# Kernel optimization log

Measured on AMD Instinct MI355X. Metric: run time of the kernel, lower is better.

## Reference

```python
import jax, jax.numpy as jnp
import numpy as np

INPUT_SIZE = 512
LABEL_NUM = 8
OUTPUT_SIZE = 64
H1 = 1024  # shared bottom width
H2 = 512   # expert hidden width
B = 8192


def setup_inputs() -> dict:
    key = jax.random.key(0)
    ks = jax.random.split(key, 8)
    s_in = 1.0 / np.sqrt(INPUT_SIZE)
    s_h1 = 1.0 / np.sqrt(H1)
    s_h2 = 1.0 / np.sqrt(H2)
    return {
        "input": jax.random.normal(ks[0], (B, INPUT_SIZE), dtype=jnp.float32),
        "category": jax.random.randint(ks[1], (B,), 0, LABEL_NUM, dtype=jnp.int32),
        # shared bottom Linear(input_size, 1024): stored as [in, out]
        "W_in": jax.random.uniform(ks[2], (INPUT_SIZE, H1), jnp.float32, -s_in, s_in),
        "b_in": jax.random.uniform(ks[3], (H1,), jnp.float32, -s_in, s_in),
        # per-expert Linear(1024, 512) stacked over experts
        "W1": jax.random.uniform(ks[4], (LABEL_NUM, H1, H2), jnp.float32, -s_h1, s_h1),
        "b1": jax.random.uniform(ks[5], (LABEL_NUM, H2), jnp.float32, -s_h1, s_h1),
        # per-expert Linear(512, output_size) stacked over experts
        "W2": jax.random.uniform(ks[6], (LABEL_NUM, H2, OUTPUT_SIZE), jnp.float32, -s_h2, s_h2),
        "b2": jax.random.uniform(ks[7], (LABEL_NUM, OUTPUT_SIZE), jnp.float32, -s_h2, s_h2),
    }


def reference(input, category, W_in, b_in, W1, b1, W2, b2):
    # Shared bottom: Linear + ELU -> [B, H1]
    mid = jax.nn.elu(input @ W_in + b_in)
    # Run all experts densely, then hard-select per-sample expert output.
    # (Faithful to per-sample hard routing; small expert count makes this clean.)
    h = jax.nn.elu(jnp.einsum("bd,edh->beh", mid, W1) + b1[None, :, :])  # [B,E,H2]
    out_all = jnp.einsum("beh,eho->beo", h, W2) + b2[None, :, :]          # [B,E,O]
    # gather the chosen expert's output for each sample
    out = jnp.take_along_axis(out_all, category[:, None, None].astype(jnp.int32).repeat(1, axis=1), axis=1)
    return out[:, 0, :]  # [B, O]
```

## Files before the change

### kernel.cpp

```cpp
#include <hip/hip_runtime.h>

typedef unsigned short u16;
typedef unsigned int u32;
typedef __bf16 bf16x8 __attribute__((ext_vector_type(8)));
typedef float f32x4 __attribute__((ext_vector_type(4)));

#define GLD_LDS(gptr, lptr) \
  __builtin_amdgcn_global_load_lds((const __attribute__((address_space(1))) void*)(gptr), \
                                   (__attribute__((address_space(3))) void*)(lptr), 16, 0, 0)

__device__ __forceinline__ u16 f2b(float f) {
  union { __bf16 h; u16 u; } v; v.h = (__bf16)f; return v.u;
}
__device__ __forceinline__ float elu1(float v) {
  return v > 0.f ? v : (__expf(v) - 1.f);
}

__device__ void transpose_tile(float (*tbuf)[65], const float* __restrict__ src,
                               u16* __restrict__ dst, int R, int C, int tr, int tc,
                               size_t zoff) {
  const int tid = threadIdx.x;
  const float* sp = src + zoff + (size_t)(tr * 64) * C + tc * 64;
#pragma unroll
  for (int i = 0; i < 4; i++) {
    const int rr = (tid >> 4) + i * 16, f = tid & 15;
    float4 v = *reinterpret_cast<const float4*>(sp + (size_t)rr * C + f * 4);
    tbuf[rr][f * 4 + 0] = v.x; tbuf[rr][f * 4 + 1] = v.y;
    tbuf[rr][f * 4 + 2] = v.z; tbuf[rr][f * 4 + 3] = v.w;
  }
  __syncthreads();
  u16* dp = dst + zoff + (size_t)(tc * 64) * R + tr * 64;
#pragma unroll
  for (int i = 0; i < 4; i++) {
    const int u = tid + i * 256;
    const int c = u >> 4, rq = u & 15;
    ushort4 w;
    w.x = f2b(tbuf[rq * 4 + 0][c]); w.y = f2b(tbuf[rq * 4 + 1][c]);
    w.z = f2b(tbuf[rq * 4 + 2][c]); w.w = f2b(tbuf[rq * 4 + 3][c]);
    *reinterpret_cast<ushort4*>(dp + (size_t)c * R + rq * 4) = w;
  }
}

__device__ void hist_body(int rb, const int* __restrict__ cat, int* __restrict__ cnts) {
  __shared__ int c8[8];
  const int tid = threadIdx.x;
  if (tid < 8) c8[tid] = 0;
  __syncthreads();
  if (tid < 128) atomicAdd(&c8[cat[rb * 128 + tid]], 1);
  __syncthreads();
  if (tid < 8) cnts[rb * 8 + tid] = c8[tid];
}

__device__ void scatter_body(int rb, const int* __restrict__ cat,
                             const int* __restrict__ cnts,
                             int* __restrict__ list, int* __restrict__ off) {
  __shared__ int lc[512];
  __shared__ int lcur[8];
  __shared__ int starts[8];
  const int tid = threadIdx.x;
  lc[tid] = cnts[tid];
  lc[tid + 256] = cnts[tid + 256];
  if (tid < 8) lcur[tid] = 0;
  __syncthreads();
  if (tid < 8) {
    const int c = tid;
    int base = 0;
    for (int cc = 0; cc < c; cc++) {
      int s = 0;
      for (int b = 0; b < 64; b++) s += lc[b * 8 + cc];
      base += s;
    }
    int pre = 0;
    for (int b = 0; b < rb; b++) pre += lc[b * 8 + c];
    starts[c] = base + pre;
    if (rb == 0) {
      off[c] = base;
      if (c == 7) {
        int s = 0;
        for (int b = 0; b < 64; b++) s += lc[b * 8 + 7];
        off[8] = base + s;
      }
    }
  }
  __syncthreads();
  if (tid < 128) {
    const int idx = rb * 128 + tid;
    const int c = cat[idx];
    const int r = atomicAdd(&lcur[c], 1);
    list[starts[c] + r] = idx;
  }
}

__global__ __launch_bounds__(256) void wsmall(const float* __restrict__ W_in,
                                              const int* __restrict__ cat,
                                              const float* __restrict__ b2,
                                              u16* __restrict__ o0, int* __restrict__ cnts,
                                              float* __restrict__ out) {
  __shared__ float tbuf[64][65];
  const int bid = blockIdx.x, tid = threadIdx.x;
  if (bid >= 192) {
    const int r = (bid - 192) * 32 + (tid >> 3);
    const int co = (tid & 7) * 8;
    const int c = cat[r];
    float4 v0 = *reinterpret_cast<const float4*>(b2 + c * 64 + co);
    float4 v1 = *reinterpret_cast<const float4*>(b2 + c * 64 + co + 4);
    *reinterpret_cast<float4*>(out + (size_t)r * 64 + co) = v0;
    *reinterpret_cast<float4*>(out + (size_t)r * 64 + co + 4) = v1;
    return;
  }
  if (bid >= 128) { hist_body(bid - 128, cat, cnts); return; }
  transpose_tile(tbuf, W_in, o0, 512, 1024, bid >> 4, bid & 15, 0);
}


template<int LAYER, int BN, int K, int N>
__global__ __launch_bounds__(256, 4) void gemm_t(
    const float* __restrict__ Xf, const u16* __restrict__ A,
    const u16* __restrict__ Bw, const float* __restrict__ bias,
    const int* __restrict__ list, const int* __restrict__ off,
    u16* __restrict__ outb, float* __restrict__ outf,
    const int* __restrict__ cat, const int* __restrict__ cnts,
    int* __restrict__ wlist, int* __restrict__ woff,
    const float* __restrict__ Wc1, const float* __restrict__ Wc2,
    u16* __restrict__ o1, u16* __restrict__ o2) {
  struct GBuf { alignas(16) u16 As[2][2048]; alignas(16) u16 Bs[2][BN * 32]; };
  __shared__ union SM {
    GBuf g;
    float tbuf[64][65];
    u16 ht[64 * 136];
  } sm;

  const int tid = threadIdx.x;

  if constexpr (LAYER == 1) {
    if (blockIdx.y == 8) {
      if (blockIdx.x < 64) scatter_body(blockIdx.x, cat, cnts, wlist, woff);
      return;
    }
    if (blockIdx.y >= 9) {
      if (blockIdx.y <= 16) {
        const int t = (blockIdx.y - 9) * 128 + blockIdx.x;
        const int z = t >> 7, rem = t & 127;
        transpose_tile(sm.tbuf, Wc1, o1, 1024, 512, rem >> 3, rem & 7,
                       (size_t)z * 1024 * 512);
      } else if (blockIdx.x < 64) {
        const int t = blockIdx.x, z = t >> 3;
        transpose_tile(sm.tbuf, Wc2, o2, 512, 64, t & 7, 0, (size_t)z * 512 * 64);
      }
      return;
    }
  }

  int tidx, col0;
  if constexpr (LAYER == 1) {
    const int orig = blockIdx.y * 128 + blockIdx.x;
    const int work = (orig & 7) * 128 + (orig >> 3);
    tidx = work >> 3;
    col0 = (work & 7) * BN;
  } else {
    const int orig = blockIdx.y * 136 + blockIdx.x;
    const int work = (orig & 7) * 68 + (orig >> 3);
    tidx = work >> 2;
    col0 = (work & 3) * BN;
  }

  const int wave = tid >> 6, lane = tid & 63;

  int e = 0, start = 0, cnt = 0, rowbase;
  if constexpr (LAYER == 1) {
    rowbase = tidx * 64;
  } else {
    int t = tidx;
    int found = -1;
    for (e = 0; e < 8; e++) {
      int tiles = (off[e + 1] - off[e] + 63) >> 6;
      if (t < tiles) { found = e; break; }
      t -= tiles;
    }
    if (found < 0) return;
    start = off[e];
    cnt = off[e + 1] - start;
    rowbase = t * 64;
  }

  const int srow = tid >> 2, skc = tid & 3;
  const int kxs = (skc ^ (srow & 3)) * 8;

  const float* ax = nullptr;
  const u16* a_src = nullptr;
  if constexpr (LAYER == 1) {
    ax = Xf + (size_t)(rowbase + srow) * K + kxs;
  } else {
    int gr = list[start + min(rowbase + srow, cnt - 1)];
    a_src = A + (size_t)gr * K + kxs;
  }
  const u16* Bbase = Bw + (LAYER == 1 ? (size_t)0 : (size_t)e * N * K);
  const u16* b_src0 = Bbase + (size_t)(col0 + srow) * K + kxs;
  const u16* b_src1 = Bbase + (size_t)(col0 + 64 + srow) * K + kxs;

  const int wbase = wave * 512;

  constexpr int NR = BN / 32;
  const int wy = wave & 1, wx = wave >> 1;
  const int fr = lane & 15, kg = lane >> 4;
  const int kx = (kg ^ (fr & 3)) * 8;
  const int ar0 = (wy * 32 + fr) * 32 + kx;
  const int br0 = (wx * (BN / 2) + fr) * 32 + kx;

  f32x4 acc[2][NR] = {};

  float4 va0, va1;
  auto LOAD_A1 = [&](int t) {
    va0 = *reinterpret_cast<const float4*>(ax + t * 32);
    va1 = *reinterpret_cast<const float4*>(ax + t * 32 + 4);
  };
  auto WRITE_A1 = [&](int buf) {
    uint4 w;
    w.x = (u32)f2b(va0.x) | ((u32)f2b(va0.y) << 16);
    w.y = (u32)f2b(va0.z) | ((u32)f2b(va0.w) << 16);
    w.z = (u32)f2b(va1.x) | ((u32)f2b(va1.y) << 16);
    w.w = (u32)f2b(va1.z) | ((u32)f2b(va1.w) << 16);
    *reinterpret_cast<uint4*>(&sm.g.As[buf][srow * 32 + skc * 8]) = w;
  };
  auto COMPUTE = [&](int buf) {
    bf16x8 af[2], bfv[NR];
#pragma unroll
    for (int m = 0; m < 2; m++) af[m] = *(const bf16x8*)&sm.g.As[buf][ar0 + m * 16 * 32];
#pragma unroll
    for (int n = 0; n < NR; n++) bfv[n] = *(const bf16x8*)&sm.g.Bs[buf][br0 + n * 16 * 32];
#pragma unroll
    for (int m = 0; m < 2; m++)
#pragma unroll
      for (int n = 0; n < NR; n++)
        acc[m][n] = __builtin_amdgcn_mfma_f32_16x16x32_bf16(af[m], bfv[n], acc[m][n], 0, 0, 0);
  };

  constexpr int NK = K / 32;
  if constexpr (LAYER == 1) LOAD_A1(0);
  else GLD_LDS(a_src, &sm.g.As[0][wbase]);
  GLD_LDS(b_src0, &sm.g.Bs[0][wbase]);
  if constexpr (BN == 128) GLD_LDS(b_src1, &sm.g.Bs[0][2048 + wbase]);
  if constexpr (LAYER == 1) WRITE_A1(0);
  __syncthreads();

  for (int it = 0; it < NK; ++it) {
    const int cur = it & 1;
    const int nxt = cur ^ 1;
    if (it + 1 < NK) {
      const int kt = (it + 1) * 32;
      if constexpr (LAYER == 1) LOAD_A1(it + 1);
      else GLD_LDS(a_src + kt, &sm.g.As[nxt][wbase]);
      GLD_LDS(b_src0 + kt, &sm.g.Bs[nxt][wbase]);
      if constexpr (BN == 128) GLD_LDS(b_src1 + kt, &sm.g.Bs[nxt][2048 + wbase]);
    }
    COMPUTE(cur);
    if constexpr (LAYER == 1) { if (it + 1 < NK) WRITE_A1(nxt); }
    __syncthreads();
  }

  if constexpr (LAYER == 1) {
#pragma unroll
    for (int n = 0; n < NR; n++) {
      const int col = col0 + wx * (BN / 2) + n * 16 + fr;
      const float bc = bias[col];
#pragma unroll
      for (int m = 0; m < 2; m++) {
        const int rloc = wy * 32 + m * 16 + kg * 4;
#pragma unroll
        for (int j = 0; j < 4; j++)
          outb[(size_t)(rowbase + rloc + j) * N + col] = f2b(elu1(acc[m][n][j] + bc));
      }
    }
  } else {
#pragma unroll
    for (int n = 0; n < NR; n++) {
      const int lcol = wx * 64 + n * 16 + fr;
      const float bc = bias[e * N + col0 + lcol];
#pragma unroll
      for (int m = 0; m < 2; m++) {
        const int rl = wy * 32 + m * 16 + kg * 4;
#pragma unroll
        for (int j = 0; j < 4; j++)
          sm.ht[(rl + j) * 136 + lcol] = f2b(elu1(acc[m][n][j] + bc));
      }
    }
    __syncthreads();

    const u16* w2p = o2 + (size_t)e * 64 * 512 + col0;
    f32x4 po[2][2] = {};
#pragma unroll
    for (int ks = 0; ks < 4; ks++) {
      bf16x8 pa[2], pb[2];
#pragma unroll
      for (int m = 0; m < 2; m++)
        pa[m] = *(const bf16x8*)&sm.ht[(wy * 32 + m * 16 + fr) * 136 + ks * 32 + kg * 8];
#pragma unroll
      for (int n = 0; n < 2; n++)
        pb[n] = *(const bf16x8*)&w2p[(size_t)(wx * 32 + n * 16 + fr) * 512 + ks * 32 + kg * 8];
#pragma unroll
      for (int m = 0; m < 2; m++)
#pragma unroll
        for (int n = 0; n < 2; n++)
          po[m][n] = __builtin_amdgcn_mfma_f32_16x16x32_bf16(pa[m], pb[n], po[m][n], 0, 0, 0);
    }
#pragma unroll
    for (int n = 0; n < 2; n++) {
      const int oc = wx * 32 + n * 16 + fr;
#pragma unroll
      for (int m = 0; m < 2; m++) {
        const int sl0 = rowbase + wy * 32 + m * 16 + kg * 4;
#pragma unroll
        for (int j = 0; j < 4; j++) {
          const int slot = sl0 + j;
          if (slot < cnt)
            atomicAdd(&outf[(size_t)list[start + slot] * 64 + oc], po[m][n][j]);
        }
      }
    }
  }
}


extern "C" void kernel_launch(void* const* d_in, const int* in_sizes, int n_in,
                              void* d_out, int out_size, void* d_ws, size_t ws_size,
                              hipStream_t stream) {
  const float* x    = (const float*)d_in[0];
  const int*   cat  = (const int*)d_in[1];
  const float* W_in = (const float*)d_in[2];
  const float* b_in = (const float*)d_in[3];
  const float* W1   = (const float*)d_in[4];
  const float* b1   = (const float*)d_in[5];
  const float* W2   = (const float*)d_in[6];
  const float* b2   = (const float*)d_in[7];
  float* out = (float*)d_out;

  char* p = (char*)d_ws;
  u16* midb = (u16*)p; p += (size_t)8192 * 1024 * 2;
  u16* wtin = (u16*)p; p += (size_t)1024 * 512 * 2;
  u16* w1t  = (u16*)p; p += (size_t)8 * 512 * 1024 * 2;
  u16* w2t  = (u16*)p; p += (size_t)8 * 64 * 512 * 2;
  int* list = (int*)p; p += (size_t)8192 * 4;
  int* off  = (int*)p; p += 64;
  int* cnts = (int*)p; p += 64 * 8 * 4;

  wsmall<<<448, 256, 0, stream>>>(W_in, cat, b2, wtin, cnts, out);

  gemm_t<1, 128, 512, 1024><<<dim3(128, 18), 256, 0, stream>>>(
      x, nullptr, wtin, b_in, nullptr, nullptr, midb, nullptr,
      cat, cnts, list, off, W1, W2, w1t, w2t);

  gemm_t<2, 128, 1024, 512><<<dim3(136, 4), 256, 0, stream>>>(
      nullptr, midb, w1t, b1, list, off, nullptr, out,
      nullptr, nullptr, nullptr, nullptr, nullptr, nullptr, nullptr, w2t);
}
```

Baseline: 59.73 us.

## Shrink layer-2 tile to 64 columns and move bias init into layer-1 kernel

The layer-2 expert GEMM now uses 64-column tiles instead of 128, splitting each expert row tile into 8 column blocks over a 1D grid of 1088 blocks, with the fused second projection reducing over 64 hidden columns per block. The output bias-initialization work moves from the small prep kernel into extra blocks of the layer-1 kernel. Smaller tiles mean more blocks for better load balance and occupancy, at the cost of more partial-output accumulation into the output, less B reuse, and extra atomics.

```diff
diff --git a/kernel.cpp b/kernel.cpp
--- a/kernel.cpp
+++ b/kernel.cpp
@@ -93,21 +93,9 @@
 
 __global__ __launch_bounds__(256) void wsmall(const float* __restrict__ W_in,
                                               const int* __restrict__ cat,
-                                              const float* __restrict__ b2,
-                                              u16* __restrict__ o0, int* __restrict__ cnts,
-                                              float* __restrict__ out) {
+                                              u16* __restrict__ o0, int* __restrict__ cnts) {
   __shared__ float tbuf[64][65];
-  const int bid = blockIdx.x, tid = threadIdx.x;
-  if (bid >= 192) {
-    const int r = (bid - 192) * 32 + (tid >> 3);
-    const int co = (tid & 7) * 8;
-    const int c = cat[r];
-    float4 v0 = *reinterpret_cast<const float4*>(b2 + c * 64 + co);
-    float4 v1 = *reinterpret_cast<const float4*>(b2 + c * 64 + co + 4);
-    *reinterpret_cast<float4*>(out + (size_t)r * 64 + co) = v0;
-    *reinterpret_cast<float4*>(out + (size_t)r * 64 + co + 4) = v1;
-    return;
-  }
+  const int bid = blockIdx.x;
   if (bid >= 128) { hist_body(bid - 128, cat, cnts); return; }
   transpose_tile(tbuf, W_in, o0, 512, 1024, bid >> 4, bid & 15, 0);
 }
@@ -122,12 +110,13 @@
     const int* __restrict__ cat, const int* __restrict__ cnts,
     int* __restrict__ wlist, int* __restrict__ woff,
     const float* __restrict__ Wc1, const float* __restrict__ Wc2,
-    u16* __restrict__ o1, u16* __restrict__ o2) {
+    u16* __restrict__ o1, u16* __restrict__ o2,
+    const float* __restrict__ b2r) {
   struct GBuf { alignas(16) u16 As[2][2048]; alignas(16) u16 Bs[2][BN * 32]; };
   __shared__ union SM {
     GBuf g;
     float tbuf[64][65];
-    u16 ht[64 * 136];
+    u16 ht[64 * 72];
   } sm;
 
   const int tid = threadIdx.x;
@@ -143,9 +132,20 @@
         const int z = t >> 7, rem = t & 127;
         transpose_tile(sm.tbuf, Wc1, o1, 1024, 512, rem >> 3, rem & 7,
                        (size_t)z * 1024 * 512);
-      } else if (blockIdx.x < 64) {
-        const int t = blockIdx.x, z = t >> 3;
-        transpose_tile(sm.tbuf, Wc2, o2, 512, 64, t & 7, 0, (size_t)z * 512 * 64);
+      } else if (blockIdx.y == 17) {
+        if (blockIdx.x < 64) {
+          const int t = blockIdx.x, z = t >> 3;
+          transpose_tile(sm.tbuf, Wc2, o2, 512, 64, t & 7, 0, (size_t)z * 512 * 64);
+        }
+      } else {
+        const int r = blockIdx.x * 64 + (tid >> 2);
+        const int co = (tid & 3) * 16;
+        const int c = cat[r];
+#pragma unroll
+        for (int q = 0; q < 4; q++) {
+          float4 v = *reinterpret_cast<const float4*>(b2r + c * 64 + co + q * 4);
+          *reinterpret_cast<float4*>(outf + (size_t)r * 64 + co + q * 4) = v;
+        }
       }
       return;
     }
@@ -158,10 +158,10 @@
     tidx = work >> 3;
     col0 = (work & 7) * BN;
   } else {
-    const int orig = blockIdx.y * 136 + blockIdx.x;
-    const int work = (orig & 7) * 68 + (orig >> 3);
-    tidx = work >> 2;
-    col0 = (work & 3) * BN;
+    const int orig = blockIdx.x;
+    const int work = (orig & 7) * 136 + (orig >> 3);
+    tidx = work;
+    col0 = 0;
   }
 
   const int wave = tid >> 6, lane = tid & 63;
@@ -173,14 +173,15 @@
     int t = tidx;
     int found = -1;
     for (e = 0; e < 8; e++) {
-      int tiles = (off[e + 1] - off[e] + 63) >> 6;
+      int tiles = (((off[e + 1] - off[e] + 63) >> 6) << 3);
       if (t < tiles) { found = e; break; }
       t -= tiles;
     }
     if (found < 0) return;
     start = off[e];
     cnt = off[e + 1] - start;
-    rowbase = t * 64;
+    rowbase = (t >> 3) * 64;
+    col0 = (t & 7) * 64;
   }
 
   const int srow = tid >> 2, skc = tid & 3;
@@ -274,14 +275,14 @@
   } else {
 #pragma unroll
     for (int n = 0; n < NR; n++) {
-      const int lcol = wx * 64 + n * 16 + fr;
+      const int lcol = wx * 32 + n * 16 + fr;
       const float bc = bias[e * N + col0 + lcol];
 #pragma unroll
       for (int m = 0; m < 2; m++) {
         const int rl = wy * 32 + m * 16 + kg * 4;
 #pragma unroll
         for (int j = 0; j < 4; j++)
-          sm.ht[(rl + j) * 136 + lcol] = f2b(elu1(acc[m][n][j] + bc));
+          sm.ht[(rl + j) * 72 + lcol] = f2b(elu1(acc[m][n][j] + bc));
       }
     }
     __syncthreads();
@@ -289,11 +290,11 @@
     const u16* w2p = o2 + (size_t)e * 64 * 512 + col0;
     f32x4 po[2][2] = {};
 #pragma unroll
-    for (int ks = 0; ks < 4; ks++) {
+    for (int ks = 0; ks < 2; ks++) {
       bf16x8 pa[2], pb[2];
 #pragma unroll
       for (int m = 0; m < 2; m++)
-        pa[m] = *(const bf16x8*)&sm.ht[(wy * 32 + m * 16 + fr) * 136 + ks * 32 + kg * 8];
+        pa[m] = *(const bf16x8*)&sm.ht[(wy * 32 + m * 16 + fr) * 72 + ks * 32 + kg * 8];
 #pragma unroll
       for (int n = 0; n < 2; n++)
         pb[n] = *(const bf16x8*)&w2p[(size_t)(wx * 32 + n * 16 + fr) * 512 + ks * 32 + kg * 8];
@@ -343,13 +344,13 @@
   int* off  = (int*)p; p += 64;
   int* cnts = (int*)p; p += 64 * 8 * 4;
 
-  wsmall<<<448, 256, 0, stream>>>(W_in, cat, b2, wtin, cnts, out);
-
-  gemm_t<1, 128, 512, 1024><<<dim3(128, 18), 256, 0, stream>>>(
-      x, nullptr, wtin, b_in, nullptr, nullptr, midb, nullptr,
-      cat, cnts, list, off, W1, W2, w1t, w2t);
-
-  gemm_t<2, 128, 1024, 512><<<dim3(136, 4), 256, 0, stream>>>(
+  wsmall<<<192, 256, 0, stream>>>(W_in, cat, wtin, cnts);
+
+  gemm_t<1, 128, 512, 1024><<<dim3(128, 19), 256, 0, stream>>>(
+      x, nullptr, wtin, b_in, nullptr, nullptr, midb, out,
+      cat, cnts, list, off, W1, W2, w1t, w2t, b2);
+
+  gemm_t<2, 64, 1024, 512><<<dim3(1088, 1), 256, 0, stream>>>(
       nullptr, midb, w1t, b1, list, off, nullptr, out,
-      nullptr, nullptr, nullptr, nullptr, nullptr, nullptr, nullptr, w2t);
-}
+      nullptr, nullptr, nullptr, nullptr, nullptr, nullptr, nullptr, w2t, nullptr);
+}
```

Result: slower. 65.99 us (+10.5%).
